# Kernel optimization log

Measured on AMD Instinct MI355X. Metric: run time of the kernel, lower is better.

Reference implementation:

```python
import jax, jax.numpy as jnp
import numpy as np

KX = jnp.array([[-1., 0., 1.], [-2., 0., 2.], [-1., 0., 1.]], dtype=jnp.float32).reshape(1, 1, 3, 3)
KY = jnp.array([[1., 2., 1.], [0., 0., 0.], [-1., -2., -1.]], dtype=jnp.float32).reshape(1, 1, 3, 3)

def _sobel(x, k):
    # x: [B,1,H,W], k: [1,1,3,3]; stride 1, padding 1 -> same spatial size
    return jax.lax.conv_general_dilated(
        x, k, window_strides=(1, 1), padding=((1, 1), (1, 1)),
        dimension_numbers=('NCHW', 'OIHW', 'NCHW'))

def setup_inputs() -> dict:
    key = jax.random.key(0)
    k1, k2 = jax.random.split(key)
    B, C, H, W = 32, 1, 512, 512
    output = jax.random.normal(k1, (B, C, H, W), dtype=jnp.float32)
    target = jax.random.normal(k2, (B, C, H, W), dtype=jnp.float32)
    return {"output": output, "target": target}

def reference(output, target):
    gx_t = _sobel(target, KX)
    gy_t = _sobel(target, KY)
    gx_o = _sobel(output, KX)
    gy_o = _sobel(output, KY)
    grad_loss = jnp.mean((gx_t - gx_o) ** 2) + jnp.mean((gy_t - gy_o) ** 2)
    return grad_loss
```

## Files before the change

kernel.cpp:

```cpp
#include <hip/hip_runtime.h>


#define BATCH 32
#define HH 512
#define WW 512
#define RW 8
#define TPB 256
#define WPI 128
#define NPART (BATCH * WPI)
#define NBLK (NPART / 4)

__global__ __launch_bounds__(TPB, 4) void sobel_partial_kernel(
    const float* __restrict__ out_img,
    const float* __restrict__ tgt_img,
    float* __restrict__ partials)
{
    const int tid  = threadIdx.x;
    const int lane = tid & 63;
    const int b    = (blockIdx.x & 7) * (NBLK / 8) + (blockIdx.x >> 3);
    const int w    = b * (TPB / 64) + (tid >> 6);
    const int img  = w >> 7;
    const int r    = w & (WPI - 1);
    const int y0   = (r >> 1) * RW;
    const int xh   = r & 1;
    const int x0   = (xh << 8) + lane * 4;

    const size_t base = (size_t)img * HH * WW;
    const float* ob = out_img + base;
    const float* tb = tgt_img + base;

    const int  seamcol = xh ? 255 : 256;
    const bool loader  = xh ? (lane == 0) : (lane == 63);

    float4 dv[RW + 2];
    float  sm[RW + 2];
    #pragma unroll
    for (int i = 0; i < RW + 2; ++i) {
        const int g = y0 - 1 + i;
        if ((unsigned)g < (unsigned)HH) {
            const size_t ro = (size_t)g * WW;
            const float4 o = *(const float4*)(ob + ro + x0);
            const float4 t = *(const float4*)(tb + ro + x0);
            dv[i] = make_float4(t.x - o.x, t.y - o.y, t.z - o.z, t.w - o.w);
            float s = 0.f;
            if (loader) s = tb[ro + seamcol] - ob[ro + seamcol];
            sm[i] = s;
        } else {
            dv[i] = make_float4(0.f, 0.f, 0.f, 0.f);
            sm[i] = 0.f;
        }
    }

    float hs[3][4], hd[3][4];
    float acc = 0.f;
    #pragma unroll
    for (int i = 0; i < RW + 2; ++i) {
        const float4 d = dv[i];
        float dl = __shfl_up(d.w, 1, 64);
        if (lane == 0)  dl = sm[i];
        float dr = __shfl_down(d.x, 1, 64);
        if (lane == 63) dr = sm[i];

        const int cur = i % 3;
        hs[cur][0] = fmaf(2.f, d.x, dl  + d.y);  hd[cur][0] = d.y - dl;
        hs[cur][1] = fmaf(2.f, d.y, d.x + d.z);  hd[cur][1] = d.z - d.x;
        hs[cur][2] = fmaf(2.f, d.z, d.y + d.w);  hd[cur][2] = d.w - d.y;
        hs[cur][3] = fmaf(2.f, d.w, d.z + dr);   hd[cur][3] = dr  - d.z;

        if (i >= 2) {
            const int top = (i - 2) % 3;
            const int mid = (i - 1) % 3;
            #pragma unroll
            for (int j = 0; j < 4; ++j) {
                const float gx = fmaf(2.f, hd[mid][j], hd[top][j] + hd[cur][j]);
                const float gy = hs[top][j] - hs[cur][j];
                acc = fmaf(gx, gx, acc);
                acc = fmaf(gy, gy, acc);
            }
        }
    }

    #pragma unroll
    for (int off = 32; off > 0; off >>= 1)
        acc += __shfl_down(acc, off, 64);
    if (lane == 0)
        partials[w] = acc;
}

__global__ __launch_bounds__(TPB) void reduce_partials_kernel(
    const float* __restrict__ partials, float* __restrict__ out)
{
    const int tid = threadIdx.x;
    float s = 0.f;
    #pragma unroll
    for (int i = 0; i < NPART / (TPB * 4); ++i) {
        const float4 v = *(const float4*)(partials + (tid + i * TPB) * 4);
        s += (v.x + v.y) + (v.z + v.w);
    }
    #pragma unroll
    for (int off = 32; off > 0; off >>= 1)
        s += __shfl_down(s, off, 64);
    __shared__ float wsum[TPB / 64];
    if ((tid & 63) == 0) wsum[tid >> 6] = s;
    __syncthreads();
    if (tid == 0)
        out[0] = (wsum[0] + wsum[1] + wsum[2] + wsum[3])
               * (1.0f / ((float)BATCH * HH * WW));
}

extern "C" void kernel_launch(void* const* d_in, const int* in_sizes, int n_in,
                              void* d_out, int out_size, void* d_ws, size_t ws_size,
                              hipStream_t stream) {
    (void)in_sizes; (void)n_in; (void)ws_size; (void)out_size;
    const float* out_img = (const float*)d_in[0];
    const float* tgt_img = (const float*)d_in[1];
    float* partials = (float*)d_ws;
    float* res = (float*)d_out;

    sobel_partial_kernel<<<NBLK, TPB, 0, stream>>>(out_img, tgt_img, partials);
    reduce_partials_kernel<<<1, TPB, 0, stream>>>(partials, res);
}
```

Baseline: 20.47 us.

## Fuse final reduction via last-block atomic counter and stream row loads

Replaces the separate reduce kernel with a last-block-done pattern: each block writes its partial sum, bumps an atomic counter, and the final block reduces all partials. Row loads become a rolling 4-slot software pipeline with clamped, branchless addressing instead of preloading all rows. Seam values are loaded once per wave across lanes and broadcast with shuffles. This saves a kernel launch and cuts register pressure, at the cost of a memset, an atomic per block, and the dropped launch-bounds occupancy hint.

```diff
diff --git a/kernel.cpp b/kernel.cpp
--- a/kernel.cpp
+++ b/kernel.cpp
@@ -5,15 +5,17 @@
 #define HH 512
 #define WW 512
 #define RW 8
+#define NR (RW + 2)
 #define TPB 256
+#define NBLK 1024
 #define WPI 128
-#define NPART (BATCH * WPI)
-#define NBLK (NPART / 4)
 
-__global__ __launch_bounds__(TPB, 4) void sobel_partial_kernel(
+__global__ __launch_bounds__(TPB) void sobel_loss_kernel(
     const float* __restrict__ out_img,
     const float* __restrict__ tgt_img,
-    float* __restrict__ partials)
+    float* __restrict__ partials,
+    unsigned* __restrict__ counter,
+    float* __restrict__ result)
 {
     const int tid  = threadIdx.x;
     const int lane = tid & 63;
@@ -28,38 +30,47 @@
     const size_t base = (size_t)img * HH * WW;
     const float* ob = out_img + base;
     const float* tb = tgt_img + base;
+    const int seamcol = xh ? 255 : 256;
 
-    const int  seamcol = xh ? 255 : 256;
-    const bool loader  = xh ? (lane == 0) : (lane == 63);
+    float seamv = 0.f;
+    if (lane < NR) {
+        const int g  = y0 - 1 + lane;
+        const int gc = min(max(g, 0), HH - 1);
+        const float m = ((unsigned)g < (unsigned)HH) ? 1.f : 0.f;
+        const size_t ro = (size_t)gc * WW + seamcol;
+        seamv = m * (tb[ro] - ob[ro]);
+    }
 
-    float4 dv[RW + 2];
-    float  sm[RW + 2];
+    float4 ro_[4], rt_[4];
+    #define LOAD_ROW(i, slot)                                              \
+        do {                                                               \
+            const int g_  = y0 - 1 + (i);                                  \
+            const int gc_ = min(max(g_, 0), HH - 1);                       \
+            const size_t off_ = (size_t)gc_ * WW + x0;                     \
+            ro_[slot] = *(const float4*)(ob + off_);                       \
+            rt_[slot] = *(const float4*)(tb + off_);                       \
+        } while (0)
+
     #pragma unroll
-    for (int i = 0; i < RW + 2; ++i) {
-        const int g = y0 - 1 + i;
-        if ((unsigned)g < (unsigned)HH) {
-            const size_t ro = (size_t)g * WW;
-            const float4 o = *(const float4*)(ob + ro + x0);
-            const float4 t = *(const float4*)(tb + ro + x0);
-            dv[i] = make_float4(t.x - o.x, t.y - o.y, t.z - o.z, t.w - o.w);
-            float s = 0.f;
-            if (loader) s = tb[ro + seamcol] - ob[ro + seamcol];
-            sm[i] = s;
-        } else {
-            dv[i] = make_float4(0.f, 0.f, 0.f, 0.f);
-            sm[i] = 0.f;
-        }
-    }
+    for (int i = 0; i < 3; ++i) LOAD_ROW(i, i);
 
     float hs[3][4], hd[3][4];
     float acc = 0.f;
     #pragma unroll
-    for (int i = 0; i < RW + 2; ++i) {
-        const float4 d = dv[i];
+    for (int i = 0; i < NR; ++i) {
+        if (i + 3 < NR) LOAD_ROW(i + 3, (i + 3) & 3);
+
+        const float4 o = ro_[i & 3];
+        const float4 t = rt_[i & 3];
+        const int   g  = y0 - 1 + i;
+        const float m  = ((unsigned)g < (unsigned)HH) ? 1.f : 0.f;
+        const float4 d = make_float4(m * (t.x - o.x), m * (t.y - o.y),
+                                     m * (t.z - o.z), m * (t.w - o.w));
+        const float sv = __shfl(seamv, i, 64);
         float dl = __shfl_up(d.w, 1, 64);
-        if (lane == 0)  dl = sm[i];
         float dr = __shfl_down(d.x, 1, 64);
-        if (lane == 63) dr = sm[i];
+        if (lane == 0)  dl = xh ? sv : 0.f;
+        if (lane == 63) dr = xh ? 0.f : sv;
 
         const int cur = i % 3;
         hs[cur][0] = fmaf(2.f, d.x, dl  + d.y);  hd[cur][0] = d.y - dl;
@@ -79,33 +90,42 @@
             }
         }
     }
+    #undef LOAD_ROW
 
     #pragma unroll
     for (int off = 32; off > 0; off >>= 1)
         acc += __shfl_down(acc, off, 64);
-    if (lane == 0)
-        partials[w] = acc;
-}
 
-__global__ __launch_bounds__(TPB) void reduce_partials_kernel(
-    const float* __restrict__ partials, float* __restrict__ out)
-{
-    const int tid = threadIdx.x;
-    float s = 0.f;
-    #pragma unroll
-    for (int i = 0; i < NPART / (TPB * 4); ++i) {
-        const float4 v = *(const float4*)(partials + (tid + i * TPB) * 4);
-        s += (v.x + v.y) + (v.z + v.w);
+    __shared__ float wsum[TPB / 64];
+    __shared__ int   lastflag;
+    if (lane == 0) wsum[tid >> 6] = acc;
+    __syncthreads();
+    if (tid == 0) {
+        const float s = wsum[0] + wsum[1] + wsum[2] + wsum[3];
+        __hip_atomic_store(&partials[b], s, __ATOMIC_RELAXED,
+                           __HIP_MEMORY_SCOPE_AGENT);
+        const unsigned old = __hip_atomic_fetch_add(counter, 1u,
+                                                    __ATOMIC_ACQ_REL,
+                                                    __HIP_MEMORY_SCOPE_AGENT);
+        lastflag = (old == NBLK - 1);
     }
-    #pragma unroll
-    for (int off = 32; off > 0; off >>= 1)
-        s += __shfl_down(s, off, 64);
-    __shared__ float wsum[TPB / 64];
-    if ((tid & 63) == 0) wsum[tid >> 6] = s;
     __syncthreads();
-    if (tid == 0)
-        out[0] = (wsum[0] + wsum[1] + wsum[2] + wsum[3])
-               * (1.0f / ((float)BATCH * HH * WW));
+
+    if (lastflag) {
+        float s = 0.f;
+        #pragma unroll
+        for (int k = 0; k < NBLK / TPB; ++k)
+            s += __hip_atomic_load(&partials[tid + k * TPB], __ATOMIC_RELAXED,
+                                   __HIP_MEMORY_SCOPE_AGENT);
+        #pragma unroll
+        for (int off = 32; off > 0; off >>= 1)
+            s += __shfl_down(s, off, 64);
+        if (lane == 0) wsum[tid >> 6] = s;
+        __syncthreads();
+        if (tid == 0)
+            result[0] = (wsum[0] + wsum[1] + wsum[2] + wsum[3])
+                      * (1.0f / ((float)BATCH * HH * WW));
+    }
 }
 
 extern "C" void kernel_launch(void* const* d_in, const int* in_sizes, int n_in,
@@ -114,9 +134,11 @@
     (void)in_sizes; (void)n_in; (void)ws_size; (void)out_size;
     const float* out_img = (const float*)d_in[0];
     const float* tgt_img = (const float*)d_in[1];
-    float* partials = (float*)d_ws;
+    float* partials  = (float*)d_ws;
+    unsigned* counter = (unsigned*)((char*)d_ws + NBLK * sizeof(float));
     float* res = (float*)d_out;
 
-    sobel_partial_kernel<<<NBLK, TPB, 0, stream>>>(out_img, tgt_img, partials);
-    reduce_partials_kernel<<<1, TPB, 0, stream>>>(partials, res);
+    hipMemsetAsync(counter, 0, sizeof(unsigned), stream);
+    sobel_loss_kernel<<<NBLK, TPB, 0, stream>>>(out_img, tgt_img,
+                                                partials, counter, res);
 }
```

Result: slower. 52.11 us (+154.6%).

## Stage full-width row tiles in LDS via async global-to-LDS copies

Applied to the files above, without the earlier changes.

Each block now handles 16 full-width rows of one image. It copies TR+2 rows of both inputs into shared memory using global_load_lds direct-to-LDS copies, then each wave computes 4 rows for both column halves from LDS. The goal is to cut the redundant halo and seam reloads from global memory and to overlap the loads asynchronously. The cost is large LDS use (about 73KB per block), which limits occupancy, plus an extra block-level reduction and a shrunken final reduce.

```diff
diff --git a/kernel.cpp b/kernel.cpp
--- a/kernel.cpp
+++ b/kernel.cpp
@@ -4,99 +4,136 @@
 #define BATCH 32
 #define HH 512
 #define WW 512
-#define RW 8
+#define TR 16
 #define TPB 256
-#define WPI 128
-#define NPART (BATCH * WPI)
-#define NBLK (NPART / 4)
+#define NBLK (BATCH * (HH / TR))
 
-__global__ __launch_bounds__(TPB, 4) void sobel_partial_kernel(
+typedef const __attribute__((address_space(1))) void* gas_ptr;
+typedef __attribute__((address_space(3))) void* las_ptr;
+
+__device__ __forceinline__ void async_copy16(const float* g, float* l) {
+    __builtin_amdgcn_global_load_lds((gas_ptr)(const void*)g,
+                                     (las_ptr)(void*)l, 16, 0, 0);
+}
+
+__global__ __launch_bounds__(TPB) void sobel_partial_kernel(
     const float* __restrict__ out_img,
     const float* __restrict__ tgt_img,
     float* __restrict__ partials)
 {
+    __shared__ float otile[TR + 2][WW];
+    __shared__ float ttile[TR + 2][WW];
+    __shared__ float wsum[TPB / 64];
+
     const int tid  = threadIdx.x;
     const int lane = tid & 63;
+    const int wv   = tid >> 6;
     const int b    = (blockIdx.x & 7) * (NBLK / 8) + (blockIdx.x >> 3);
-    const int w    = b * (TPB / 64) + (tid >> 6);
-    const int img  = w >> 7;
-    const int r    = w & (WPI - 1);
-    const int y0   = (r >> 1) * RW;
-    const int xh   = r & 1;
-    const int x0   = (xh << 8) + lane * 4;
+    const int img  = b >> 5;
+    const int y0   = (b & 31) * TR;
 
     const size_t base = (size_t)img * HH * WW;
-    const float* ob = out_img + base;
-    const float* tb = tgt_img + base;
 
-    const int  seamcol = xh ? 255 : 256;
-    const bool loader  = xh ? (lane == 0) : (lane == 63);
+    const int top    = (y0 == 0);
+    const int bot    = (y0 + TR == HH);
+    const int srcRow0 = top ? 0 : y0 - 1;
+    const int ldsRow0 = top ? 1 : 0;
+    const int nchunk  = (TR + 2 - top - bot) * 2;
+    const float* osrc = out_img + base + (size_t)srcRow0 * WW;
+    const float* tsrc = tgt_img + base + (size_t)srcRow0 * WW;
+    float* old = &otile[ldsRow0][0];
+    float* tld = &ttile[ldsRow0][0];
+    for (int c = wv; c < nchunk; c += 4) {
+        const int off = c * 256 + lane * 4;
+        async_copy16(osrc + off, old + off);
+        async_copy16(tsrc + off, tld + off);
+    }
+    if (top) {
+        if (tid < 128) *(float4*)&otile[0][tid * 4] = make_float4(0, 0, 0, 0);
+        else           *(float4*)&ttile[0][(tid - 128) * 4] = make_float4(0, 0, 0, 0);
+    }
+    if (bot) {
+        if (tid < 128) *(float4*)&otile[TR + 1][tid * 4] = make_float4(0, 0, 0, 0);
+        else           *(float4*)&ttile[TR + 1][(tid - 128) * 4] = make_float4(0, 0, 0, 0);
+    }
+    __syncthreads();
 
-    float4 dv[RW + 2];
-    float  sm[RW + 2];
-    #pragma unroll
-    for (int i = 0; i < RW + 2; ++i) {
-        const int g = y0 - 1 + i;
-        if ((unsigned)g < (unsigned)HH) {
-            const size_t ro = (size_t)g * WW;
-            const float4 o = *(const float4*)(ob + ro + x0);
-            const float4 t = *(const float4*)(tb + ro + x0);
-            dv[i] = make_float4(t.x - o.x, t.y - o.y, t.z - o.z, t.w - o.w);
-            float s = 0.f;
-            if (loader) s = tb[ro + seamcol] - ob[ro + seamcol];
-            sm[i] = s;
-        } else {
-            dv[i] = make_float4(0.f, 0.f, 0.f, 0.f);
-            sm[i] = 0.f;
-        }
+    float s255 = 0.f, s256 = 0.f;
+    if (lane < TR + 2) {
+        s255 = ttile[lane][255] - otile[lane][255];
+        s256 = ttile[lane][256] - otile[lane][256];
     }
 
-    float hs[3][4], hd[3][4];
+    const int R0 = 4 * wv;
     float acc = 0.f;
+
+#define ROWLOAD(dst, R)                                                     \
+    {                                                                       \
+        const float4 o4 = *(const float4*)&otile[(R)][cb];                  \
+        const float4 t4 = *(const float4*)&ttile[(R)][cb];                  \
+        dst = make_float4(t4.x - o4.x, t4.y - o4.y, t4.z - o4.z, t4.w - o4.w); \
+    }
+#define ROWPASS(hs, hd, d, R)                                               \
+    {                                                                       \
+        const float svL = __shfl(s255, (R), 64);                            \
+        const float svR = __shfl(s256, (R), 64);                            \
+        float dl = __shfl_up((d).w, 1, 64);                                 \
+        float dr = __shfl_down((d).x, 1, 64);                               \
+        if (lane == 0)  dl = h ? svL : 0.f;                                 \
+        if (lane == 63) dr = h ? 0.f : svR;                                 \
+        hs.x = fmaf(2.f, (d).x, dl + (d).y);      hd.x = (d).y - dl;        \
+        hs.y = fmaf(2.f, (d).y, (d).x + (d).z);   hd.y = (d).z - (d).x;     \
+        hs.z = fmaf(2.f, (d).z, (d).y + (d).w);   hd.z = (d).w - (d).y;     \
+        hs.w = fmaf(2.f, (d).w, (d).z + dr);      hd.w = dr - (d).z;        \
+    }
+#define ACCUM(hsT, hdT, hsM, hdM, hsB, hdB)                                 \
+    {                                                                       \
+        float gx, gy;                                                       \
+        gx = fmaf(2.f, hdM.x, hdT.x + hdB.x); gy = hsT.x - hsB.x;           \
+        acc = fmaf(gx, gx, acc); acc = fmaf(gy, gy, acc);                   \
+        gx = fmaf(2.f, hdM.y, hdT.y + hdB.y); gy = hsT.y - hsB.y;           \
+        acc = fmaf(gx, gx, acc); acc = fmaf(gy, gy, acc);                   \
+        gx = fmaf(2.f, hdM.z, hdT.z + hdB.z); gy = hsT.z - hsB.z;           \
+        acc = fmaf(gx, gx, acc); acc = fmaf(gy, gy, acc);                   \
+        gx = fmaf(2.f, hdM.w, hdT.w + hdB.w); gy = hsT.w - hsB.w;           \
+        acc = fmaf(gx, gx, acc); acc = fmaf(gy, gy, acc);                   \
+    }
+
     #pragma unroll
-    for (int i = 0; i < RW + 2; ++i) {
-        const float4 d = dv[i];
-        float dl = __shfl_up(d.w, 1, 64);
-        if (lane == 0)  dl = sm[i];
-        float dr = __shfl_down(d.x, 1, 64);
-        if (lane == 63) dr = sm[i];
-
-        const int cur = i % 3;
-        hs[cur][0] = fmaf(2.f, d.x, dl  + d.y);  hd[cur][0] = d.y - dl;
-        hs[cur][1] = fmaf(2.f, d.y, d.x + d.z);  hd[cur][1] = d.z - d.x;
-        hs[cur][2] = fmaf(2.f, d.z, d.y + d.w);  hd[cur][2] = d.w - d.y;
-        hs[cur][3] = fmaf(2.f, d.w, d.z + dr);   hd[cur][3] = dr  - d.z;
-
-        if (i >= 2) {
-            const int top = (i - 2) % 3;
-            const int mid = (i - 1) % 3;
-            #pragma unroll
-            for (int j = 0; j < 4; ++j) {
-                const float gx = fmaf(2.f, hd[mid][j], hd[top][j] + hd[cur][j]);
-                const float gy = hs[top][j] - hs[cur][j];
-                acc = fmaf(gx, gx, acc);
-                acc = fmaf(gy, gy, acc);
-            }
-        }
+    for (int h = 0; h < 2; ++h) {
+        const int cb = (h << 8) + lane * 4;
+        float4 d0, d1, d2;
+        float4 hs0, hd0, hs1, hd1, hs2, hd2;
+        ROWLOAD(d0, R0 + 0); ROWPASS(hs0, hd0, d0, R0 + 0);
+        ROWLOAD(d1, R0 + 1); ROWPASS(hs1, hd1, d1, R0 + 1);
+        ROWLOAD(d2, R0 + 2); ROWPASS(hs2, hd2, d2, R0 + 2);
+        ACCUM(hs0, hd0, hs1, hd1, hs2, hd2);
+        ROWLOAD(d0, R0 + 3); ROWPASS(hs0, hd0, d0, R0 + 3);
+        ACCUM(hs1, hd1, hs2, hd2, hs0, hd0);
+        ROWLOAD(d1, R0 + 4); ROWPASS(hs1, hd1, d1, R0 + 4);
+        ACCUM(hs2, hd2, hs0, hd0, hs1, hd1);
+        ROWLOAD(d2, R0 + 5); ROWPASS(hs2, hd2, d2, R0 + 5);
+        ACCUM(hs0, hd0, hs1, hd1, hs2, hd2);
     }
+#undef ROWLOAD
+#undef ROWPASS
+#undef ACCUM
 
     #pragma unroll
     for (int off = 32; off > 0; off >>= 1)
         acc += __shfl_down(acc, off, 64);
-    if (lane == 0)
-        partials[w] = acc;
+    if (lane == 0) wsum[wv] = acc;
+    __syncthreads();
+    if (tid == 0)
+        partials[b] = wsum[0] + wsum[1] + wsum[2] + wsum[3];
 }
 
 __global__ __launch_bounds__(TPB) void reduce_partials_kernel(
     const float* __restrict__ partials, float* __restrict__ out)
 {
     const int tid = threadIdx.x;
-    float s = 0.f;
-    #pragma unroll
-    for (int i = 0; i < NPART / (TPB * 4); ++i) {
-        const float4 v = *(const float4*)(partials + (tid + i * TPB) * 4);
-        s += (v.x + v.y) + (v.z + v.w);
-    }
+    const float4 v = *(const float4*)(partials + tid * 4);
+    float s = (v.x + v.y) + (v.z + v.w);
     #pragma unroll
     for (int off = 32; off > 0; off >>= 1)
         s += __shfl_down(s, off, 64);
```

After: 19.72 us. 1.04x faster.

## Give each wave full 512-wide rows over 4-row strips with 8 columns per lane

Applied to the files above, without the earlier changes.

Each wave now covers a full image row width, with every lane holding 8 columns as two float4 loads. This removes the seam-column extra loads at the half-row boundary. The strip height drops from 8 to 4 rows, which raises the halo overhead from 10/8 to 6/4 rows loaded. Loads are clamped and then masked instead of branched. Partials are reduced per block through shared memory, so the final kernel only sums 1024 values.

```diff
diff --git a/kernel.cpp b/kernel.cpp
--- a/kernel.cpp
+++ b/kernel.cpp
@@ -4,99 +4,113 @@
 #define BATCH 32
 #define HH 512
 #define WW 512
-#define RW 8
+#define RW 4
 #define TPB 256
-#define WPI 128
-#define NPART (BATCH * WPI)
-#define NBLK (NPART / 4)
+#define NBLK 1024
+#define SPI (HH / RW)
 
-__global__ __launch_bounds__(TPB, 4) void sobel_partial_kernel(
+__global__ __launch_bounds__(TPB) void sobel_partial_kernel(
     const float* __restrict__ out_img,
     const float* __restrict__ tgt_img,
     float* __restrict__ partials)
 {
     const int tid  = threadIdx.x;
     const int lane = tid & 63;
+    const int wv   = tid >> 6;
     const int b    = (blockIdx.x & 7) * (NBLK / 8) + (blockIdx.x >> 3);
-    const int w    = b * (TPB / 64) + (tid >> 6);
+    const int w    = b * (TPB / 64) + wv;
     const int img  = w >> 7;
-    const int r    = w & (WPI - 1);
-    const int y0   = (r >> 1) * RW;
-    const int xh   = r & 1;
-    const int x0   = (xh << 8) + lane * 4;
+    const int y0   = (w & (SPI - 1)) * RW;
+    const size_t base = (size_t)img * HH * WW;
+    const float* ob = out_img + base + (lane << 3);
+    const float* tb = tgt_img + base + (lane << 3);
 
-    const size_t base = (size_t)img * HH * WW;
-    const float* ob = out_img + base;
-    const float* tb = tgt_img + base;
+    float acc = 0.f;
 
-    const int  seamcol = xh ? 255 : 256;
-    const bool loader  = xh ? (lane == 0) : (lane == 63);
+#define DECLROW(j) float4 oA##j, oB##j, tA##j, tB##j, dA##j, dB##j,            \
+                          hsA##j, hdA##j, hsB##j, hdB##j;
 
-    float4 dv[RW + 2];
-    float  sm[RW + 2];
-    #pragma unroll
-    for (int i = 0; i < RW + 2; ++i) {
-        const int g = y0 - 1 + i;
-        if ((unsigned)g < (unsigned)HH) {
-            const size_t ro = (size_t)g * WW;
-            const float4 o = *(const float4*)(ob + ro + x0);
-            const float4 t = *(const float4*)(tb + ro + x0);
-            dv[i] = make_float4(t.x - o.x, t.y - o.y, t.z - o.z, t.w - o.w);
-            float s = 0.f;
-            if (loader) s = tb[ro + seamcol] - ob[ro + seamcol];
-            sm[i] = s;
-        } else {
-            dv[i] = make_float4(0.f, 0.f, 0.f, 0.f);
-            sm[i] = 0.f;
-        }
-    }
+#define LOADR(j) {                                                             \
+    const int gc = min(max(y0 - 1 + (j), 0), HH - 1);                          \
+    const float* orow_ = ob + (size_t)gc * WW;                                 \
+    const float* trow_ = tb + (size_t)gc * WW;                                 \
+    oA##j = *(const float4*)orow_;       oB##j = *(const float4*)(orow_ + 4);  \
+    tA##j = *(const float4*)trow_;       tB##j = *(const float4*)(trow_ + 4);  }
 
-    float hs[3][4], hd[3][4];
-    float acc = 0.f;
-    #pragma unroll
-    for (int i = 0; i < RW + 2; ++i) {
-        const float4 d = dv[i];
-        float dl = __shfl_up(d.w, 1, 64);
-        if (lane == 0)  dl = sm[i];
-        float dr = __shfl_down(d.x, 1, 64);
-        if (lane == 63) dr = sm[i];
+#define DIFFH(j) {                                                             \
+    const float m_ = ((unsigned)(y0 - 1 + (j)) < (unsigned)HH) ? 1.f : 0.f;    \
+    dA##j = make_float4(m_*(tA##j.x-oA##j.x), m_*(tA##j.y-oA##j.y),            \
+                        m_*(tA##j.z-oA##j.z), m_*(tA##j.w-oA##j.w));           \
+    dB##j = make_float4(m_*(tB##j.x-oB##j.x), m_*(tB##j.y-oB##j.y),            \
+                        m_*(tB##j.z-oB##j.z), m_*(tB##j.w-oB##j.w));           \
+    float dl_ = __shfl_up(dB##j.w, 1, 64);   if (lane == 0)  dl_ = 0.f;        \
+    float dr_ = __shfl_down(dA##j.x, 1, 64); if (lane == 63) dr_ = 0.f;        \
+    hsA##j.x = fmaf(2.f, dA##j.x, dl_ + dA##j.y);                              \
+    hdA##j.x = dA##j.y - dl_;                                                  \
+    hsA##j.y = fmaf(2.f, dA##j.y, dA##j.x + dA##j.z);                          \
+    hdA##j.y = dA##j.z - dA##j.x;                                              \
+    hsA##j.z = fmaf(2.f, dA##j.z, dA##j.y + dA##j.w);                          \
+    hdA##j.z = dA##j.w - dA##j.y;                                              \
+    hsA##j.w = fmaf(2.f, dA##j.w, dA##j.z + dB##j.x);                          \
+    hdA##j.w = dB##j.x - dA##j.z;                                              \
+    hsB##j.x = fmaf(2.f, dB##j.x, dA##j.w + dB##j.y);                          \
+    hdB##j.x = dB##j.y - dA##j.w;                                              \
+    hsB##j.y = fmaf(2.f, dB##j.y, dB##j.x + dB##j.z);                          \
+    hdB##j.y = dB##j.z - dB##j.x;                                              \
+    hsB##j.z = fmaf(2.f, dB##j.z, dB##j.y + dB##j.w);                          \
+    hdB##j.z = dB##j.w - dB##j.y;                                              \
+    hsB##j.w = fmaf(2.f, dB##j.w, dB##j.z + dr_);                              \
+    hdB##j.w = dr_ - dB##j.z;                                                  }
 
-        const int cur = i % 3;
-        hs[cur][0] = fmaf(2.f, d.x, dl  + d.y);  hd[cur][0] = d.y - dl;
-        hs[cur][1] = fmaf(2.f, d.y, d.x + d.z);  hd[cur][1] = d.z - d.x;
-        hs[cur][2] = fmaf(2.f, d.z, d.y + d.w);  hd[cur][2] = d.w - d.y;
-        hs[cur][3] = fmaf(2.f, d.w, d.z + dr);   hd[cur][3] = dr  - d.z;
+#define VP1(S, a, bb, c) {                                                     \
+    float gx_, gy_;                                                            \
+    gx_ = fmaf(2.f, hd##S##bb.x, hd##S##a.x + hd##S##c.x);                     \
+    gy_ = hs##S##a.x - hs##S##c.x;                                             \
+    acc = fmaf(gx_, gx_, acc); acc = fmaf(gy_, gy_, acc);                      \
+    gx_ = fmaf(2.f, hd##S##bb.y, hd##S##a.y + hd##S##c.y);                     \
+    gy_ = hs##S##a.y - hs##S##c.y;                                             \
+    acc = fmaf(gx_, gx_, acc); acc = fmaf(gy_, gy_, acc);                      \
+    gx_ = fmaf(2.f, hd##S##bb.z, hd##S##a.z + hd##S##c.z);                     \
+    gy_ = hs##S##a.z - hs##S##c.z;                                             \
+    acc = fmaf(gx_, gx_, acc); acc = fmaf(gy_, gy_, acc);                      \
+    gx_ = fmaf(2.f, hd##S##bb.w, hd##S##a.w + hd##S##c.w);                     \
+    gy_ = hs##S##a.w - hs##S##c.w;                                             \
+    acc = fmaf(gx_, gx_, acc); acc = fmaf(gy_, gy_, acc);                      }
+#define VPASS(a, bb, c) VP1(A, a, bb, c) VP1(B, a, bb, c)
 
-        if (i >= 2) {
-            const int top = (i - 2) % 3;
-            const int mid = (i - 1) % 3;
-            #pragma unroll
-            for (int j = 0; j < 4; ++j) {
-                const float gx = fmaf(2.f, hd[mid][j], hd[top][j] + hd[cur][j]);
-                const float gy = hs[top][j] - hs[cur][j];
-                acc = fmaf(gx, gx, acc);
-                acc = fmaf(gy, gy, acc);
-            }
-        }
-    }
+    DECLROW(0) DECLROW(1) DECLROW(2) DECLROW(3) DECLROW(4) DECLROW(5)
+
+    LOADR(0) LOADR(1) LOADR(2) LOADR(3)
+    DIFFH(0) DIFFH(1)
+    LOADR(4)
+    DIFFH(2) VPASS(0, 1, 2)
+    LOADR(5)
+    DIFFH(3) VPASS(1, 2, 3)
+    DIFFH(4) VPASS(2, 3, 4)
+    DIFFH(5) VPASS(3, 4, 5)
+
+#undef DECLROW
+#undef LOADR
+#undef DIFFH
+#undef VP1
+#undef VPASS
 
     #pragma unroll
     for (int off = 32; off > 0; off >>= 1)
         acc += __shfl_down(acc, off, 64);
-    if (lane == 0)
-        partials[w] = acc;
+    __shared__ float wsum[TPB / 64];
+    if (lane == 0) wsum[wv] = acc;
+    __syncthreads();
+    if (tid == 0)
+        partials[b] = wsum[0] + wsum[1] + wsum[2] + wsum[3];
 }
 
 __global__ __launch_bounds__(TPB) void reduce_partials_kernel(
     const float* __restrict__ partials, float* __restrict__ out)
 {
     const int tid = threadIdx.x;
-    float s = 0.f;
-    #pragma unroll
-    for (int i = 0; i < NPART / (TPB * 4); ++i) {
-        const float4 v = *(const float4*)(partials + (tid + i * TPB) * 4);
-        s += (v.x + v.y) + (v.z + v.w);
-    }
+    const float4 v = *(const float4*)(partials + tid * 4);
+    float s = (v.x + v.y) + (v.z + v.w);
     #pragma unroll
     for (int off = 32; off > 0; off >>= 1)
         s += __shfl_down(s, off, 64);
```

Result: faster. 18.62 us (-9.0%).
